# Kernel optimization log

Measured on AMD Instinct MI355X. Metric: run time of the kernel, lower is better.

The kernel has to match this reference:

```python
import jax, jax.numpy as jnp
import numpy as np

B, T, C, HS = 8, 2048, 1024, 128

def setup_inputs() -> dict:
    key = jax.random.key(0)
    kx, kq, kk, kv = jax.random.split(key, 4)
    x = jax.random.normal(kx, (B, T, C), dtype=jnp.float32)
    # torch Linear(C, HS, bias=False): y = x @ W^T with W [HS, C].
    # We store the transposed form [C, HS] and right-multiply (same math).
    scale = 1.0 / np.sqrt(C)  # torch default init scale-ish; exact init irrelevant for correctness
    Wq = jax.random.normal(kq, (C, HS), dtype=jnp.float32) * scale
    Wk = jax.random.normal(kk, (C, HS), dtype=jnp.float32) * scale
    Wv = jax.random.normal(kv, (C, HS), dtype=jnp.float32) * scale
    return {"x": x, "Wq": Wq, "Wk": Wk, "Wv": Wv}

def reference(x, Wq, Wk, Wv):
    Bx, Tx, Cx = x.shape
    q = x @ Wq  # [B, T, HS]
    k = x @ Wk
    v = x @ Wv
    # NOTE: original scales by C**-0.5 where C = n_embd (not head_size)
    wei = jnp.einsum('btd,bsd->bts', q, k) * (Cx ** -0.5)  # [B, T, T]
    causal = jnp.tril(jnp.ones((Tx, Tx), dtype=bool))
    wei = jnp.where(causal, wei, -jnp.inf)
    wei = jax.nn.softmax(wei, axis=-1)
    # dropout rate 0.0 (eval semantics) -> identity
    return jnp.einsum('bts,bsd->btd', wei, v)  # [B, T, HS]
```

## Files before the change

### kernel.cpp

```cpp
#include <hip/hip_runtime.h>
#include <hip/hip_bf16.h>
#include <stdint.h>

typedef float f32x4 __attribute__((ext_vector_type(4)));
typedef float f32x4v __attribute__((ext_vector_type(4)));
typedef short short8 __attribute__((ext_vector_type(8)));
typedef unsigned short u16;
typedef unsigned short u16x8 __attribute__((ext_vector_type(8)));
typedef unsigned short u16x4 __attribute__((ext_vector_type(4)));

#define MFMA16x16x32 __builtin_amdgcn_mfma_f32_16x16x32_bf16

__device__ __forceinline__ u16 f2bf(float f) {
    unsigned int u = __builtin_bit_cast(unsigned int, f);
    u += 0x7fffu + ((u >> 16) & 1u);
    return (u16)(u >> 16);
}

__device__ __forceinline__ void gload_lds16(const void* g, void* l) {
    __builtin_amdgcn_global_load_lds(
        (const __attribute__((address_space(1))) uint32_t*)g,
        (__attribute__((address_space(3))) uint32_t*)l, 16, 0, 0);
}

__device__ __forceinline__ int z_small(int na) {
    int za = (8 * na + 32) / 33;
    return za < 1 ? 1 : za;
}

__global__ void k_transpose_wf(const float* __restrict__ Wq, const float* __restrict__ Wk,
                               const float* __restrict__ Wv, u16* __restrict__ WTf) {
    int tid  = blockIdx.x * 256 + threadIdx.x;
    int f    = tid >> 6;
    int lane = tid & 63;
    int kt  = f / 48;
    int rem = f % 48;
    int ks  = rem / 24;
    int nc  = rem % 24;
    int col = nc * 16 + (lane & 15);
    int w   = col >> 7, n = col & 127;
    int k0  = kt * 64 + ks * 32 + (lane >> 4) * 8;
    const float* W = (w == 0) ? Wq : ((w == 1) ? Wk : Wv);
    u16x8 v;
#pragma unroll
    for (int j = 0; j < 8; ++j)
        v[j] = f2bf(W[(size_t)(k0 + j) * 128 + n]);
    *(u16x8*)(&WTf[(size_t)tid * 8]) = v;
}

__global__ __launch_bounds__(512) void k_qkv_gemm8(
    const float* __restrict__ x, const u16* __restrict__ WTf,
    u16* __restrict__ qb, u16* __restrict__ kb, u16* __restrict__ vT)
{
    __shared__ u16 abuf[2][64 * 64];
    __shared__ u16 bbuf[2][384 * 64];
    const int tid  = threadIdx.x;
    const int lane = tid & 63, wid = tid >> 6;
    const int wr = wid >> 2, wc = wid & 3;
    const int lrow = lane & 15, lk = lane >> 4;
    const int m0 = blockIdx.x * 64;

    const int arow = tid >> 3;
    const int aseg = tid & 7;
    const float* xsrc = x + (size_t)(m0 + arow) * 1024 + aseg * 8;

    f32x4 acc[2][6];
#pragma unroll
    for (int i = 0; i < 2; ++i)
#pragma unroll
        for (int j = 0; j < 6; ++j) acc[i][j] = (f32x4){0.f, 0.f, 0.f, 0.f};

#define LOADA(s0, s1, ktv)                                                     \
    s0 = *(const f32x4v*)(xsrc + (ktv) * 64);                                  \
    s1 = *(const f32x4v*)(xsrc + (ktv) * 64 + 4);

#define STOREA(buf, s0, s1)                                                    \
    {   u16x8 v;                                                               \
        v[0]=f2bf(s0[0]); v[1]=f2bf(s0[1]); v[2]=f2bf(s0[2]); v[3]=f2bf(s0[3]); \
        v[4]=f2bf(s1[0]); v[5]=f2bf(s1[1]); v[6]=f2bf(s1[2]); v[7]=f2bf(s1[3]); \
        *(u16x8*)(&buf[arow * 64 + ((aseg ^ (arow & 7)) << 3)]) = v; }

#define ISSUEB(buf, ktv)                                                       \
    {   const u16* bsrc = WTf + (size_t)(ktv) * 24576;                         \
        _Pragma("unroll") for (int i = 0; i < 6; ++i) {                        \
            int c = tid + i * 512;                                             \
            gload_lds16(bsrc + c * 8, &buf[c * 8]);                            \
        } }

#define COMPUTE(ab, bb)                                                        \
    _Pragma("unroll") for (int ks = 0; ks < 2; ++ks) {                         \
        short8 af[2];                                                          \
        _Pragma("unroll") for (int mf = 0; mf < 2; ++mf) {                     \
            int row = wr * 32 + mf * 16 + lrow;                                \
            int blk = (ks * 4 + lk) ^ (row & 7);                               \
            af[mf] = *(const short8*)(&ab[row * 64 + (blk << 3)]);             \
        }                                                                      \
        _Pragma("unroll") for (int nf = 0; nf < 6; ++nf) {                     \
            short8 bfr = *(const short8*)(&bb[(ks * 24 + wc * 6 + nf) * 512 + lane * 8]); \
            _Pragma("unroll") for (int mf = 0; mf < 2; ++mf)                   \
                acc[mf][nf] = MFMA16x16x32(af[mf], bfr, acc[mf][nf], 0, 0, 0); \
        } }

#define WAITBAR()                                                              \
    asm volatile("s_waitcnt vmcnt(2) lgkmcnt(0)\n\ts_barrier" ::: "memory");   \
    __builtin_amdgcn_sched_barrier(0);

    f32x4v a0A, a1A, a0B, a1B;
    LOADA(a0A, a1A, 0);
    LOADA(a0B, a1B, 1);
    STOREA(abuf[0], a0A, a1A);
    ISSUEB(bbuf[0], 0);
    LOADA(a0A, a1A, 2);
    WAITBAR();

    for (int kt = 0; kt < 16; kt += 2) {
        {
            const int ktn = (kt + 1 < 16) ? kt + 1 : 15;
            ISSUEB(bbuf[1], ktn);
            __builtin_amdgcn_sched_barrier(0);
            COMPUTE(abuf[0], bbuf[0]);
            STOREA(abuf[1], a0B, a1B);
            const int kp = (kt + 3 < 16) ? kt + 3 : 15;
            LOADA(a0B, a1B, kp);
            WAITBAR();
        }
        {
            const int ktn = (kt + 2 < 16) ? kt + 2 : 15;
            ISSUEB(bbuf[0], ktn);
            __builtin_amdgcn_sched_barrier(0);
            COMPUTE(abuf[1], bbuf[1]);
            STOREA(abuf[0], a0A, a1A);
            const int kp = (kt + 4 < 16) ? kt + 4 : 15;
            LOADA(a0A, a1A, kp);
            WAITBAR();
        }
    }
#undef LOADA
#undef STOREA
#undef ISSUEB
#undef COMPUTE
#undef WAITBAR

#pragma unroll
    for (int nf = 0; nf < 6; ++nf) {
        const int gc   = wc * 96 + nf * 16 + lrow;
        const int wsel = gc >> 7;
        const int col  = gc & 127;
#pragma unroll
        for (int mf = 0; mf < 2; ++mf) {
            const int row0 = m0 + wr * 32 + mf * 16 + lk * 4;
            if (wsel == 0) {
#pragma unroll
                for (int jj = 0; jj < 4; ++jj)
                    qb[(size_t)(row0 + jj) * 128 + col] = f2bf(acc[mf][nf][jj]);
            } else if (wsel == 1) {
#pragma unroll
                for (int jj = 0; jj < 4; ++jj)
                    kb[(size_t)(row0 + jj) * 128 + col] = f2bf(acc[mf][nf][jj]);
            } else {
                const int bb = row0 >> 11, t0 = row0 & 2047;
                u16x4 v;
#pragma unroll
                for (int jj = 0; jj < 4; ++jj) v[jj] = f2bf(acc[mf][nf][jj]);
                *(u16x4*)(&vT[((size_t)bb * 128 + col) * 2048 + t0]) = v;
            }
        }
    }
}

__global__ __launch_bounds__(256) void k_flash7(
    const u16* __restrict__ qb, const u16* __restrict__ kb, const u16* __restrict__ vT,
    float* __restrict__ po, float* __restrict__ pm, float* __restrict__ pl)
{
    __shared__ u16 k_lds[2][64 * 128];
    __shared__ u16 v_lds[2][128 * 64];
    __shared__ u16 p_lds[4 * 16 * 64];
    const int tid  = threadIdx.x;
    const int lane = tid & 63, wid = tid >> 6;
    const int lrow = lane & 15, lk = lane >> 4;
    const int bx = blockIdx.x;
    const int b  = bx & 7;
    const int p  = (bx >> 3) & 15;
    const int z  = bx >> 7;

    const int na = p + 1;
    const int za = z_small(na);
    int qt, n, k, Z;
    if (z < za) { qt = p;      n = na;     k = z;      Z = za;     }
    else        { qt = 31 - p; n = 32 - p; k = z - za; Z = 8 - za; }
    const int t0 = (k * n) / Z;
    const int t1 = ((k + 1) * n) / Z;

    const int qrow0 = qt * 64;
    short8 qf[4];
    {
        const u16* qp = qb + ((size_t)b * 2048 + qrow0 + wid * 16 + lrow) * 128;
#pragma unroll
        for (int ks = 0; ks < 4; ++ks) qf[ks] = *(const short8*)(qp + ks * 32 + lk * 8);
    }
    f32x4 of[8];
#pragma unroll
    for (int i = 0; i < 8; ++i) of[i] = (f32x4){0.f, 0.f, 0.f, 0.f};
    float mrun[4], lsum[4];
#pragma unroll
    for (int j = 0; j < 4; ++j) { mrun[j] = -1e30f; lsum[j] = 0.f; }

    const u16* kbase = kb + (size_t)b * 2048 * 128;
    const u16* vbase = vT + (size_t)b * 128 * 2048;
    u16* pw = p_lds + wid * (16 * 64);

#define ISSUE_KV(c_, t_)                                                       \
    {   const int kv0_ = (t_) << 6;                                            \
        _Pragma("unroll") for (int i = 0; i < 4; ++i) {                        \
            int ch = tid + i * 256;                                            \
            int row = ch >> 4, blk = ch & 15;                                  \
            gload_lds16(kbase + (size_t)(kv0_ + row) * 128 + ((blk ^ (row & 7)) << 3), \
                        &k_lds[c_][ch * 8]);                                   \
        }                                                                      \
        _Pragma("unroll") for (int i = 0; i < 4; ++i) {                        \
            int ch = tid + i * 256;                                            \
            int row = ch >> 3, blk = ch & 7;                                   \
            gload_lds16(vbase + (size_t)row * 2048 + kv0_ + ((blk ^ (row & 7)) << 3), \
                        &v_lds[c_][ch * 8]);                                   \
        }                                                                      \
        __builtin_amdgcn_sched_barrier(0); }

    ISSUE_KV(0, t0);
    int c = 0;

    for (int t = t0; t < t1; ++t) {
        asm volatile("s_waitcnt vmcnt(0) lgkmcnt(0)\n\ts_barrier" ::: "memory");
        __builtin_amdgcn_sched_barrier(0);
        if (t + 1 < t1) ISSUE_KV(c ^ 1, t + 1);

        f32x4 sf[4];
#pragma unroll
        for (int nf = 0; nf < 4; ++nf) sf[nf] = (f32x4){0.f, 0.f, 0.f, 0.f};
#pragma unroll
        for (int ks = 0; ks < 4; ++ks)
#pragma unroll
            for (int nf = 0; nf < 4; ++nf) {
                int row = nf * 16 + lrow;
                int blk = (ks * 4 + lk) ^ (row & 7);
                short8 bfr = *(const short8*)(&k_lds[c][row * 128 + (blk << 3)]);
                sf[nf] = MFMA16x16x32(qf[ks], bfr, sf[nf], 0, 0, 0);
            }

        const bool diag = (t == n - 1);
#pragma unroll
        for (int nf = 0; nf < 4; ++nf)
#pragma unroll
            for (int jj = 0; jj < 4; ++jj) {
                float s = sf[nf][jj] * 0.03125f;
                if (diag && (nf * 16 + lrow > wid * 16 + lk * 4 + jj)) s = -1e30f;
                sf[nf][jj] = s;
            }
        float mt[4];
#pragma unroll
        for (int jj = 0; jj < 4; ++jj)
            mt[jj] = fmaxf(fmaxf(sf[0][jj], sf[1][jj]), fmaxf(sf[2][jj], sf[3][jj]));
#pragma unroll
        for (int off = 1; off < 16; off <<= 1)
#pragma unroll
            for (int jj = 0; jj < 4; ++jj)
                mt[jj] = fmaxf(mt[jj], __shfl_xor(mt[jj], off));
        bool small = true;
#pragma unroll
        for (int jj = 0; jj < 4; ++jj) small = small && (mt[jj] <= mrun[jj] + 8.f);
        if (!__all(small)) {
#pragma unroll
            for (int jj = 0; jj < 4; ++jj) {
                float mnew = fmaxf(mrun[jj], mt[jj]);
                float sc   = __expf(mrun[jj] - mnew);
                mrun[jj]   = mnew;
                lsum[jj]  *= sc;
#pragma unroll
                for (int df = 0; df < 8; ++df) of[df][jj] *= sc;
            }
        }
        float rs[4] = {0.f, 0.f, 0.f, 0.f};
#pragma unroll
        for (int nf = 0; nf < 4; ++nf)
#pragma unroll
            for (int jj = 0; jj < 4; ++jj) {
                float e = __expf(sf[nf][jj] - mrun[jj]);
                sf[nf][jj] = e;
                rs[jj] += e;
            }
#pragma unroll
        for (int off = 1; off < 16; off <<= 1)
#pragma unroll
            for (int jj = 0; jj < 4; ++jj)
                rs[jj] += __shfl_xor(rs[jj], off);
#pragma unroll
        for (int jj = 0; jj < 4; ++jj) lsum[jj] += rs[jj];

#pragma unroll
        for (int nf = 0; nf < 4; ++nf)
#pragma unroll
            for (int jj = 0; jj < 4; ++jj) {
                int row = lk * 4 + jj;
                int col = nf * 16 + lrow;
                pw[row * 64 + (((col >> 3) ^ (row & 7)) << 3) + (col & 7)] = f2bf(sf[nf][jj]);
            }
        asm volatile("s_waitcnt lgkmcnt(0)" ::: "memory");
        __builtin_amdgcn_sched_barrier(0);
        short8 paf[2];
#pragma unroll
        for (int ks2 = 0; ks2 < 2; ++ks2) {
            int blk = (ks2 * 4 + lk) ^ (lrow & 7);
            paf[ks2] = *(const short8*)(&pw[lrow * 64 + (blk << 3)]);
        }
#pragma unroll
        for (int ks2 = 0; ks2 < 2; ++ks2)
#pragma unroll
            for (int df = 0; df < 8; ++df) {
                int row = df * 16 + lrow;
                int blk = (ks2 * 4 + lk) ^ (row & 7);
                short8 vf = *(const short8*)(&v_lds[c][row * 64 + (blk << 3)]);
                of[df] = MFMA16x16x32(paf[ks2], vf, of[df], 0, 0, 0);
            }
        c ^= 1;
    }
#undef ISSUE_KV

    float* poslab = po + (size_t)bx * (64 * 128);
#pragma unroll
    for (int df = 0; df < 8; ++df)
#pragma unroll
        for (int jj = 0; jj < 4; ++jj)
            poslab[(size_t)(wid * 16 + lk * 4 + jj) * 128 + df * 16 + lrow] = of[df][jj];
    if (lrow == 0) {
#pragma unroll
        for (int jj = 0; jj < 4; ++jj) {
            pm[(size_t)bx * 64 + wid * 16 + lk * 4 + jj] = mrun[jj];
            pl[(size_t)bx * 64 + wid * 16 + lk * 4 + jj] = lsum[jj];
        }
    }
}

__global__ __launch_bounds__(256) void k_combine(
    const float* __restrict__ po, const float* __restrict__ pm, const float* __restrict__ pl,
    float* __restrict__ out)
{
    const int row  = blockIdx.x * 4 + (threadIdx.x >> 6);
    const int lane = threadIdx.x & 63;
    const int b  = row >> 11;
    const int t  = row & 2047;
    const int qt = t >> 6;
    const int r  = t & 63;

    const int p  = (qt < 16) ? qt : 31 - qt;
    const int za = z_small(p + 1);
    const int zlo = (qt < 16) ? 0 : za;
    const int zhi = (qt < 16) ? za : 8;

    float M = -1e30f;
    for (int z = zlo; z < zhi; ++z)
        M = fmaxf(M, pm[(size_t)(b + 8 * p + 128 * z) * 64 + r]);
    float den = 0.f, a0 = 0.f, a1 = 0.f;
    for (int z = zlo; z < zhi; ++z) {
        const int bxp = b + 8 * p + 128 * z;
        const float w = __expf(pm[(size_t)bxp * 64 + r] - M);
        den += w * pl[(size_t)bxp * 64 + r];
        const float* slab = po + ((size_t)bxp * 64 + r) * 128;
        a0 += w * slab[lane];
        a1 += w * slab[lane + 64];
    }
    const float inv = 1.f / den;
    out[(size_t)row * 128 + lane]      = a0 * inv;
    out[(size_t)row * 128 + lane + 64] = a1 * inv;
}

extern "C" void kernel_launch(void* const* d_in, const int* in_sizes, int n_in,
                              void* d_out, int out_size, void* d_ws, size_t ws_size,
                              hipStream_t stream) {
    const float* x  = (const float*)d_in[0];
    const float* Wq = (const float*)d_in[1];
    const float* Wk = (const float*)d_in[2];
    const float* Wv = (const float*)d_in[3];
    float* out = (float*)d_out;

    char* ws = (char*)d_ws;
    u16*   qb  = (u16*)(ws);
    u16*   kb  = (u16*)(ws + (size_t)4  * 1048576);
    u16*   vT  = (u16*)(ws + (size_t)8  * 1048576);
    u16*   WTf = (u16*)(ws + (size_t)12 * 1048576);
    float* po  = (float*)(ws + (size_t)13 * 1048576);
    float* pm  = (float*)(ws + (size_t)47 * 1048576);
    float* pl  = (float*)(ws + (size_t)48 * 1048576);

    k_transpose_wf<<<192, 256, 0, stream>>>(Wq, Wk, Wv, WTf);
    k_qkv_gemm8<<<256, 512, 0, stream>>>(x, WTf, qb, kb, vT);
    k_flash7<<<1024, 256, 0, stream>>>(qb, kb, vT, po, pm, pl);
    k_combine<<<4096, 256, 0, stream>>>(po, pm, pl, out);
}
```

Before: 76.67 us.

## Retile QKV GEMM to 128-row tiles per projection and store partials in bf16

```diff
diff --git a/kernel.cpp b/kernel.cpp
--- a/kernel.cpp
+++ b/kernel.cpp
@@ -15,6 +15,10 @@
     unsigned int u = __builtin_bit_cast(unsigned int, f);
     u += 0x7fffu + ((u >> 16) & 1u);
     return (u16)(u >> 16);
+}
+__device__ __forceinline__ float bf2f(u16 v) {
+    unsigned int u = ((unsigned int)v) << 16;
+    return __builtin_bit_cast(float, u);
 }
 
 __device__ __forceinline__ void gload_lds16(const void* g, void* l) {
@@ -48,121 +52,105 @@
     *(u16x8*)(&WTf[(size_t)tid * 8]) = v;
 }
 
-__global__ __launch_bounds__(512) void k_qkv_gemm8(
+__global__ __launch_bounds__(256) void k_qkv_gemm11(
     const float* __restrict__ x, const u16* __restrict__ WTf,
     u16* __restrict__ qb, u16* __restrict__ kb, u16* __restrict__ vT)
 {
-    __shared__ u16 abuf[2][64 * 64];
-    __shared__ u16 bbuf[2][384 * 64];
+    __shared__ u16 la[128 * 64];
+    __shared__ u16 bb[2 * 8 * 512];
     const int tid  = threadIdx.x;
     const int lane = tid & 63, wid = tid >> 6;
-    const int wr = wid >> 2, wc = wid & 3;
+    const int wr = wid >> 1, wc = wid & 1;
     const int lrow = lane & 15, lk = lane >> 4;
-    const int m0 = blockIdx.x * 64;
-
-    const int arow = tid >> 3;
-    const int aseg = tid & 7;
-    const float* xsrc = x + (size_t)(m0 + arow) * 1024 + aseg * 8;
-
-    f32x4 acc[2][6];
-#pragma unroll
-    for (int i = 0; i < 2; ++i)
-#pragma unroll
-        for (int j = 0; j < 6; ++j) acc[i][j] = (f32x4){0.f, 0.f, 0.f, 0.f};
-
-#define LOADA(s0, s1, ktv)                                                     \
-    s0 = *(const f32x4v*)(xsrc + (ktv) * 64);                                  \
-    s1 = *(const f32x4v*)(xsrc + (ktv) * 64 + 4);
-
-#define STOREA(buf, s0, s1)                                                    \
-    {   u16x8 v;                                                               \
-        v[0]=f2bf(s0[0]); v[1]=f2bf(s0[1]); v[2]=f2bf(s0[2]); v[3]=f2bf(s0[3]); \
-        v[4]=f2bf(s1[0]); v[5]=f2bf(s1[1]); v[6]=f2bf(s1[2]); v[7]=f2bf(s1[3]); \
-        *(u16x8*)(&buf[arow * 64 + ((aseg ^ (arow & 7)) << 3)]) = v; }
-
-#define ISSUEB(buf, ktv)                                                       \
-    {   const u16* bsrc = WTf + (size_t)(ktv) * 24576;                         \
-        _Pragma("unroll") for (int i = 0; i < 6; ++i) {                        \
-            int c = tid + i * 512;                                             \
-            gload_lds16(bsrc + c * 8, &buf[c * 8]);                            \
+    const int bx   = blockIdx.x;
+    const int mlo  = bx & 7;
+    const int rest = bx >> 3;
+    const int nt   = rest % 3;
+    const int m0   = ((rest / 3) * 8 + mlo) * 128;
+
+    const int ar   = tid >> 1;
+    const int aseg = tid & 1;
+    const float* xsrc = x + (size_t)(m0 + ar) * 1024 + aseg * 32;
+
+    f32x4 acc[4][4];
+#pragma unroll
+    for (int i = 0; i < 4; ++i)
+#pragma unroll
+        for (int j = 0; j < 4; ++j) acc[i][j] = (f32x4){0.f, 0.f, 0.f, 0.f};
+
+    f32x4v pa[8];
+#define LOADA(ktv)                                                             \
+    _Pragma("unroll") for (int j = 0; j < 8; ++j)                              \
+        pa[j] = *(const f32x4v*)(xsrc + (ktv) * 64 + j * 4);
+
+#define STOREA()                                                               \
+    _Pragma("unroll") for (int j = 0; j < 4; ++j) {                            \
+        u16x8 v;                                                               \
+        v[0]=f2bf(pa[2*j][0]); v[1]=f2bf(pa[2*j][1]);                          \
+        v[2]=f2bf(pa[2*j][2]); v[3]=f2bf(pa[2*j][3]);                          \
+        v[4]=f2bf(pa[2*j+1][0]); v[5]=f2bf(pa[2*j+1][1]);                      \
+        v[6]=f2bf(pa[2*j+1][2]); v[7]=f2bf(pa[2*j+1][3]);                      \
+        *(u16x8*)(&la[ar * 64 + (((aseg * 4 + j) ^ (ar & 7)) << 3)]) = v;      \
+    }
+
+#define ISSUEB(ktv)                                                            \
+    {   _Pragma("unroll") for (int i = 0; i < 4; ++i) {                        \
+            int c   = tid + i * 256;                              \
+            int ks_ = c >> 9;                                                  \
+            int r_  = c & 511;                                                 \
+            const u16* src = WTf + ((size_t)(((ktv) * 2 + ks_) * 24 + nt * 8   \
+                                    + (r_ >> 6)) * 512 + (r_ & 63) * 8);       \
+            gload_lds16(src, &bb[c * 8]);                                      \
         } }
 
-#define COMPUTE(ab, bb)                                                        \
+#define COMPUTE()                                                              \
     _Pragma("unroll") for (int ks = 0; ks < 2; ++ks) {                         \
-        short8 af[2];                                                          \
-        _Pragma("unroll") for (int mf = 0; mf < 2; ++mf) {                     \
-            int row = wr * 32 + mf * 16 + lrow;                                \
+        short8 af[4];                                                          \
+        _Pragma("unroll") for (int mf = 0; mf < 4; ++mf) {                     \
+            int row = wr * 64 + mf * 16 + lrow;                                \
             int blk = (ks * 4 + lk) ^ (row & 7);                               \
-            af[mf] = *(const short8*)(&ab[row * 64 + (blk << 3)]);             \
+            af[mf] = *(const short8*)(&la[row * 64 + (blk << 3)]);             \
         }                                                                      \
-        _Pragma("unroll") for (int nf = 0; nf < 6; ++nf) {                     \
-            short8 bfr = *(const short8*)(&bb[(ks * 24 + wc * 6 + nf) * 512 + lane * 8]); \
-            _Pragma("unroll") for (int mf = 0; mf < 2; ++mf)                   \
+        _Pragma("unroll") for (int nf = 0; nf < 4; ++nf) {                     \
+            short8 bfr = *(const short8*)(&bb[(ks * 8 + wc * 4 + nf) * 512 + lane * 8]); \
+            _Pragma("unroll") for (int mf = 0; mf < 4; ++mf)                   \
                 acc[mf][nf] = MFMA16x16x32(af[mf], bfr, acc[mf][nf], 0, 0, 0); \
         } }
 
-#define WAITBAR()                                                              \
-    asm volatile("s_waitcnt vmcnt(2) lgkmcnt(0)\n\ts_barrier" ::: "memory");   \
-    __builtin_amdgcn_sched_barrier(0);
-
-    f32x4v a0A, a1A, a0B, a1B;
-    LOADA(a0A, a1A, 0);
-    LOADA(a0B, a1B, 1);
-    STOREA(abuf[0], a0A, a1A);
-    ISSUEB(bbuf[0], 0);
-    LOADA(a0A, a1A, 2);
-    WAITBAR();
-
-    for (int kt = 0; kt < 16; kt += 2) {
-        {
-            const int ktn = (kt + 1 < 16) ? kt + 1 : 15;
-            ISSUEB(bbuf[1], ktn);
-            __builtin_amdgcn_sched_barrier(0);
-            COMPUTE(abuf[0], bbuf[0]);
-            STOREA(abuf[1], a0B, a1B);
-            const int kp = (kt + 3 < 16) ? kt + 3 : 15;
-            LOADA(a0B, a1B, kp);
-            WAITBAR();
-        }
-        {
-            const int ktn = (kt + 2 < 16) ? kt + 2 : 15;
-            ISSUEB(bbuf[0], ktn);
-            __builtin_amdgcn_sched_barrier(0);
-            COMPUTE(abuf[1], bbuf[1]);
-            STOREA(abuf[0], a0A, a1A);
-            const int kp = (kt + 4 < 16) ? kt + 4 : 15;
-            LOADA(a0A, a1A, kp);
-            WAITBAR();
-        }
+    LOADA(0);
+    for (int kt = 0; kt < 16; ++kt) {
+        __syncthreads();
+        STOREA();
+        ISSUEB(kt);
+        __syncthreads();
+        if (kt + 1 < 16) LOADA(kt + 1);
+        COMPUTE();
     }
 #undef LOADA
 #undef STOREA
 #undef ISSUEB
 #undef COMPUTE
-#undef WAITBAR
-
-#pragma unroll
-    for (int nf = 0; nf < 6; ++nf) {
-        const int gc   = wc * 96 + nf * 16 + lrow;
-        const int wsel = gc >> 7;
-        const int col  = gc & 127;
-#pragma unroll
-        for (int mf = 0; mf < 2; ++mf) {
-            const int row0 = m0 + wr * 32 + mf * 16 + lk * 4;
-            if (wsel == 0) {
+
+#pragma unroll
+    for (int nf = 0; nf < 4; ++nf) {
+        const int col = wc * 64 + nf * 16 + lrow;
+#pragma unroll
+        for (int mf = 0; mf < 4; ++mf) {
+            const int row0 = m0 + wr * 64 + mf * 16 + lk * 4;
+            if (nt == 0) {
 #pragma unroll
                 for (int jj = 0; jj < 4; ++jj)
                     qb[(size_t)(row0 + jj) * 128 + col] = f2bf(acc[mf][nf][jj]);
-            } else if (wsel == 1) {
+            } else if (nt == 1) {
 #pragma unroll
                 for (int jj = 0; jj < 4; ++jj)
                     kb[(size_t)(row0 + jj) * 128 + col] = f2bf(acc[mf][nf][jj]);
             } else {
-                const int bb = row0 >> 11, t0 = row0 & 2047;
+                const int bb2 = row0 >> 11, t0 = row0 & 2047;
                 u16x4 v;
 #pragma unroll
                 for (int jj = 0; jj < 4; ++jj) v[jj] = f2bf(acc[mf][nf][jj]);
-                *(u16x4*)(&vT[((size_t)bb * 128 + col) * 2048 + t0]) = v;
+                *(u16x4*)(&vT[((size_t)bb2 * 128 + col) * 2048 + t0]) = v;
             }
         }
     }
@@ -170,7 +158,7 @@
 
 __global__ __launch_bounds__(256) void k_flash7(
     const u16* __restrict__ qb, const u16* __restrict__ kb, const u16* __restrict__ vT,
-    float* __restrict__ po, float* __restrict__ pm, float* __restrict__ pl)
+    u16* __restrict__ po, float* __restrict__ pm, float* __restrict__ pl)
 {
     __shared__ u16 k_lds[2][64 * 128];
     __shared__ u16 v_lds[2][128 * 64];
@@ -324,12 +312,12 @@
     }
 #undef ISSUE_KV
 
-    float* poslab = po + (size_t)bx * (64 * 128);
+    u16* poslab = po + (size_t)bx * (64 * 128);
 #pragma unroll
     for (int df = 0; df < 8; ++df)
 #pragma unroll
         for (int jj = 0; jj < 4; ++jj)
-            poslab[(size_t)(wid * 16 + lk * 4 + jj) * 128 + df * 16 + lrow] = of[df][jj];
+            poslab[(size_t)(wid * 16 + lk * 4 + jj) * 128 + df * 16 + lrow] = f2bf(of[df][jj]);
     if (lrow == 0) {
 #pragma unroll
         for (int jj = 0; jj < 4; ++jj) {
@@ -340,7 +328,7 @@
 }
 
 __global__ __launch_bounds__(256) void k_combine(
-    const float* __restrict__ po, const float* __restrict__ pm, const float* __restrict__ pl,
+    const u16* __restrict__ po, const float* __restrict__ pm, const float* __restrict__ pl,
     float* __restrict__ out)
 {
     const int row  = blockIdx.x * 4 + (threadIdx.x >> 6);
@@ -363,9 +351,9 @@
         const int bxp = b + 8 * p + 128 * z;
         const float w = __expf(pm[(size_t)bxp * 64 + r] - M);
         den += w * pl[(size_t)bxp * 64 + r];
-        const float* slab = po + ((size_t)bxp * 64 + r) * 128;
-        a0 += w * slab[lane];
-        a1 += w * slab[lane + 64];
+        const u16* slab = po + ((size_t)bxp * 64 + r) * 128;
+        a0 += w * bf2f(slab[lane]);
+        a1 += w * bf2f(slab[lane + 64]);
     }
     const float inv = 1.f / den;
     out[(size_t)row * 128 + lane]      = a0 * inv;
@@ -386,12 +374,12 @@
     u16*   kb  = (u16*)(ws + (size_t)4  * 1048576);
     u16*   vT  = (u16*)(ws + (size_t)8  * 1048576);
     u16*   WTf = (u16*)(ws + (size_t)12 * 1048576);
-    float* po  = (float*)(ws + (size_t)13 * 1048576);
+    u16*   po  = (u16*)(ws + (size_t)13 * 1048576);
     float* pm  = (float*)(ws + (size_t)47 * 1048576);
     float* pl  = (float*)(ws + (size_t)48 * 1048576);
 
     k_transpose_wf<<<192, 256, 0, stream>>>(Wq, Wk, Wv, WTf);
-    k_qkv_gemm8<<<256, 512, 0, stream>>>(x, WTf, qb, kb, vT);
+    k_qkv_gemm11<<<384, 256, 0, stream>>>(x, WTf, qb, kb, vT);
     k_flash7<<<1024, 256, 0, stream>>>(qb, kb, vT, po, pm, pl);
     k_combine<<<4096, 256, 0, stream>>>(po, pm, pl, out);
 }
```

After: 100.3 us. 30.9% more time.
